# Optimization experiments

Measured on AMD Instinct MI355X. Metric: run time of the kernel, lower is better.

The kernel has to match this reference:

```python
import jax, jax.numpy as jnp
import numpy as np
from jax import lax

DYADIC_ORDER = 0
NAIVE_SOLVER = False


def _increments(X, Y):
    # Linear static kernel Gram: (A, M, N)
    G = jnp.einsum('amd,and->amn', X, Y)
    # Second-order finite-difference increments: (A, M-1, N-1)
    inc = G[:, 1:, 1:] + G[:, :-1, :-1] - G[:, 1:, :-1] - G[:, :-1, 1:]
    f = 2 ** DYADIC_ORDER
    if f > 1:
        # torch `tile` with index_select == consecutive repeat == jnp.repeat
        inc = jnp.repeat(jnp.repeat(inc, f, axis=1), f, axis=2) / float(f * f)
    return inc


def _sig_kernel(X, Y):
    """Signature-kernel PDE solve. X:(A,M,D), Y:(A,N,D) -> (A,)"""
    inc = _increments(X, Y)            # (A, MM, NN)
    A, MM, NN = inc.shape

    def row_step(prev_row, g_row):
        # prev_row: (A, NN+1) = K[i, :];  g_row: (A, NN) = G[:, i, :]
        def col_step(k_left, inp):
            k00, k01, g = inp          # each (A,)
            if NAIVE_SOLVER:
                k_new = k_left + k01 + k00 * (g - 1.0)
            else:
                k_new = (k_left + k01) * (1.0 + 0.5 * g + g * g / 12.0) \
                        - k00 * (1.0 - g * g / 12.0)
            return k_new, k_new

        xs = (prev_row[:, :-1].T, prev_row[:, 1:].T, g_row.T)  # (NN, A) each
        _, tail = lax.scan(col_step, jnp.ones((A,), inc.dtype), xs)
        new_row = jnp.concatenate([jnp.ones((A, 1), inc.dtype), tail.T], axis=1)
        return new_row, None

    init_row = jnp.ones((A, NN + 1), inc.dtype)  # K[0, :] = 1
    final_row, _ = lax.scan(row_step, init_row, jnp.moveaxis(inc, 1, 0))
    return final_row[:, -1]            # K[:, MM, NN]


def setup_inputs() -> dict:
    key = jax.random.key(0)
    kx, ky = jax.random.split(key)
    A, M, D = 128, 256, 16
    # scale 0.1 keeps Gram increments small so the PDE stays stable
    X = 0.1 * jax.random.normal(kx, (A, M, D), dtype=jnp.float32)
    Y = 0.1 * jax.random.normal(ky, (A, M, D), dtype=jnp.float32)
    return {"X": X, "Y": Y}


def reference(X, Y):
    k_XX = _sig_kernel(X, X)
    k_YY = _sig_kernel(Y, Y)
    k_XY = _sig_kernel(X, Y)
    return jnp.mean(k_XX) + jnp.mean(k_YY) - 2.0 * jnp.mean(k_XY)
```

## Files before the change

### kernel.cpp

```cpp
#include <hip/hip_runtime.h>

typedef float f32x2 __attribute__((ext_vector_type(2)));

#define NA   128
#define NPTS 256
#define DD   16
#define MMI  255
#define NSTEP (MMI + 63)

__device__ __forceinline__ float wave_shr1(float x, float boundary) {
    int r = __builtin_amdgcn_update_dpp(
        __builtin_bit_cast(int, boundary),
        __builtin_bit_cast(int, x),
        0x138 , 0xF, 0xF, false);
    return __builtin_bit_cast(float, r);
}

__global__ __launch_bounds__(64)
void sig_pde(const float* __restrict__ X, const float* __restrict__ Y,
             float* __restrict__ out) {
    const int pid  = blockIdx.x;
    const int pair = pid >> 7;
    const int a    = pid & 127;
    const float* U = (pair == 1) ? Y : X;
    const float* V = (pair == 0) ? X : Y;
    const float  w = (pair == 2) ? (-2.0f / (float)NA) : (1.0f / (float)NA);
    U += (size_t)a * (NPTS * DD);
    V += (size_t)a * (NPTS * DD);

    __shared__ float dU[4][256][4];

    const int lane = threadIdx.x;

    const float4* U4 = (const float4*)U;
    #pragma unroll
    for (int i = 0; i < 16; ++i) {
        int t  = lane + (i << 6);
        int qd = t >> 8;
        int r  = t & 255;
        float4 val = make_float4(0.f, 0.f, 0.f, 0.f);
        if (r < MMI) {
            float4 lo = U4[r * 4 + qd];
            float4 hi = U4[r * 4 + 4 + qd];
            val = make_float4(hi.x - lo.x, hi.y - lo.y, hi.z - lo.z, hi.w - lo.w);
        }
        *(float4*)(&dU[qd][r][0]) = val;
    }

    f32x2 v[4][8];
    #pragma unroll
    for (int k = 0; k < 4; ++k) {
        int j = (lane << 2) + k;
        const bool valid = (j < MMI);
        const int jj = valid ? j : 0;
        const float2* Va = (const float2*)(V + (size_t)jj * DD);
        const float2* Vb = (const float2*)(V + (size_t)(jj + 1) * DD);
        #pragma unroll
        for (int q = 0; q < 8; ++q) {
            float2 lo = Va[q], hi = Vb[q];
            v[k][q] = valid ? f32x2{hi.x - lo.x, hi.y - lo.y} : f32x2{0.f, 0.f};
        }
    }

    __syncthreads();

    auto rowidx = [&](int s) {
        int rr = s - lane;
        return ((unsigned)rr < (unsigned)MMI) ? rr : 255;
    };
    auto load_row = [&](int s, f32x2* uu) {
        const float4* p = (const float4*)&dU[0][rowidx(s)][0];
        #pragma unroll
        for (int q = 0; q < 4; ++q) {
            float4 t = p[q << 8];
            uu[2 * q + 0] = f32x2{t.x, t.y};
            uu[2 * q + 1] = f32x2{t.z, t.w};
        }
    };

    float c1[4], c2[4];
    auto compute_c = [&](const f32x2* uu) {
        #pragma unroll
        for (int k = 0; k < 4; ++k) {
            f32x2 acc = uu[0] * v[k][0];
            #pragma unroll
            for (int q = 1; q < 8; ++q) acc += uu[q] * v[k][q];
            const float g = acc.x + acc.y;
            const float e = g * g * (1.0f / 12.0f);
            c1[k] = fmaf(0.5f, g, 1.0f) + e;
            c2[k] = 1.0f - e;
        }
    };

    float kup0 = 1.f, kup1 = 1.f, kup2 = 1.f, kup3 = 1.f;
    float shnew = 1.f, shprev = 1.f;

    auto step = [&]() {
        const float left   = shnew;
        const float upleft = shprev;
        const float pre0 = fmaf(kup0, c1[0], -(upleft * c2[0]));
        const float pre1 = fmaf(kup1, c1[1], -(kup0 * c2[1]));
        const float pre2 = fmaf(kup2, c1[2], -(kup1 * c2[2]));
        const float pre3 = fmaf(kup3, c1[3], -(kup2 * c2[3]));
        const float t0 = fmaf(left, c1[0], pre0);
        const float t1 = fmaf(t0,   c1[1], pre1);
        const float t2 = fmaf(t1,   c1[2], pre2);
        const float t3 = fmaf(t2,   c1[3], pre3);
        shprev = shnew;
        kup0 = t0; kup1 = t1; kup2 = t2; kup3 = t3;
        shnew = wave_shr1(t3, 1.0f);
    };

    f32x2 bufA[8], bufB[8], bufC[8];
    {
        f32x2 t[8];
        load_row(0, t);
        compute_c(t);
    }
    load_row(1, bufA);
    load_row(2, bufB);

    for (int s = 0; s < NSTEP; s += 3) {
        load_row(s + 3, bufC);
        step();
        compute_c(bufA);

        load_row(s + 4, bufA);
        step();
        compute_c(bufB);

        load_row(s + 5, bufB);
        step();
        compute_c(bufC);
    }

    if (lane == 63) atomicAdd(out, w * kup2);
}

extern "C" void kernel_launch(void* const* d_in, const int* in_sizes, int n_in,
                              void* d_out, int out_size, void* d_ws, size_t ws_size,
                              hipStream_t stream) {
    const float* X = (const float*)d_in[0];
    const float* Y = (const float*)d_in[1];
    float* out = (float*)d_out;
    hipMemsetAsync(out, 0, sizeof(float), stream);
    sig_pde<<<dim3(3 * NA), dim3(64), 0, stream>>>(X, Y, out);
}
```

Baseline: 112.5 us.

## Precompute skewed Gram increments in fp16 workspace before the PDE sweep

Splits the work into two kernels. A parallel kernel computes all Gram increments in anti-diagonal (skewed) order and stores them as fp16 in the workspace. A lean wavefront kernel then streams them from global memory with a 6-deep prefetch, so the serial PDE loop no longer does the 16-wide dot products. This trades an extra kernel launch and global memory traffic for a shorter serial critical path. Storing increments in fp16 adds precision risk, and the original single kernel remains as a fallback when the workspace is too small.

```diff
diff --git a/kernel.cpp b/kernel.cpp
--- a/kernel.cpp
+++ b/kernel.cpp
@@ -1,12 +1,16 @@
 #include <hip/hip_runtime.h>
+#include <hip/hip_fp16.h>
 
 typedef float f32x2 __attribute__((ext_vector_type(2)));
 
-#define NA   128
-#define NPTS 256
-#define DD   16
-#define MMI  255
-#define NSTEP (MMI + 63)
+#define NA    128
+#define NPTS  256
+#define DD    16
+#define MMI   255
+#define NSTEP 318
+#define GROWS 318
+#define G_ELEMS ((size_t)3 * NA * GROWS * 256)
+#define G_BYTES (G_ELEMS * 2)
 
 __device__ __forceinline__ float wave_shr1(float x, float boundary) {
     int r = __builtin_amdgcn_update_dpp(
@@ -14,6 +18,137 @@
         __builtin_bit_cast(int, x),
         0x138 , 0xF, 0xF, false);
     return __builtin_bit_cast(float, r);
+}
+
+__global__ __launch_bounds__(256)
+void sig_gram(const float* __restrict__ X, const float* __restrict__ Y,
+              __half* __restrict__ G) {
+    const int bx    = blockIdx.x;
+    const int pb    = bx >> 2;
+    const int chunk = bx & 3;
+    const int pair  = pb >> 7;
+    const int a     = pb & 127;
+    const float* U = (pair == 1) ? Y : X;
+    const float* V = (pair == 0) ? X : Y;
+    U += (size_t)a * (NPTS * DD);
+    V += (size_t)a * (NPTS * DD);
+
+    __shared__ float dU[4][256][4];
+    __shared__ float dV[4][256][4];
+
+    const int tid = threadIdx.x;
+
+    const float4* U4 = (const float4*)U;
+    const float4* V4 = (const float4*)V;
+    #pragma unroll
+    for (int q = 0; q < 4; ++q) {
+        float4 uval = make_float4(0.f, 0.f, 0.f, 0.f);
+        float4 vval = make_float4(0.f, 0.f, 0.f, 0.f);
+        if (tid < MMI) {
+            float4 lo = U4[tid * 4 + q], hi = U4[tid * 4 + 4 + q];
+            uval = make_float4(hi.x - lo.x, hi.y - lo.y, hi.z - lo.z, hi.w - lo.w);
+            lo = V4[tid * 4 + q]; hi = V4[tid * 4 + 4 + q];
+            vval = make_float4(hi.x - lo.x, hi.y - lo.y, hi.z - lo.z, hi.w - lo.w);
+        }
+        *(float4*)(&dU[q][tid][0]) = uval;
+        *(float4*)(&dV[q][tid][0]) = vval;
+    }
+    __syncthreads();
+
+    f32x2 v[8];
+    #pragma unroll
+    for (int q = 0; q < 4; ++q) {
+        float4 t = *(const float4*)(&dV[q][tid][0]);
+        v[2 * q + 0] = f32x2{t.x, t.y};
+        v[2 * q + 1] = f32x2{t.z, t.w};
+    }
+
+    const int s0beg = 80 * chunk;
+    const int s0end = (s0beg + 80 < GROWS) ? s0beg + 80 : GROWS;
+    int rr = s0beg - (tid >> 2);
+    __half* gp = G + (size_t)pb * (GROWS * 256) + (size_t)s0beg * 256 + tid;
+
+    for (int s0 = s0beg; s0 < s0end; ++s0) {
+        int rc = rr < 0 ? 0 : (rr > 255 ? 255 : rr);
+        f32x2 acc;
+        {
+            float4 t0 = *(const float4*)(&dU[0][rc][0]);
+            float4 t1 = *(const float4*)(&dU[1][rc][0]);
+            float4 t2 = *(const float4*)(&dU[2][rc][0]);
+            float4 t3 = *(const float4*)(&dU[3][rc][0]);
+            acc = f32x2{t0.x, t0.y} * v[0];
+            acc = __builtin_elementwise_fma(f32x2{t0.z, t0.w}, v[1], acc);
+            acc = __builtin_elementwise_fma(f32x2{t1.x, t1.y}, v[2], acc);
+            acc = __builtin_elementwise_fma(f32x2{t1.z, t1.w}, v[3], acc);
+            acc = __builtin_elementwise_fma(f32x2{t2.x, t2.y}, v[4], acc);
+            acc = __builtin_elementwise_fma(f32x2{t2.z, t2.w}, v[5], acc);
+            acc = __builtin_elementwise_fma(f32x2{t3.x, t3.y}, v[6], acc);
+            acc = __builtin_elementwise_fma(f32x2{t3.z, t3.w}, v[7], acc);
+        }
+        float g = acc.x + acc.y;
+        g = (rr < 0) ? 0.f : g;
+        *gp = __float2half(g);
+        gp += 256;
+        ++rr;
+    }
+}
+
+__global__ __launch_bounds__(64)
+void sig_pde2(const __half* __restrict__ G, float* __restrict__ out) {
+    const int pid  = blockIdx.x;
+    const int pair = pid >> 7;
+    const float w  = (pair == 2) ? (-2.0f / (float)NA) : (1.0f / (float)NA);
+    const int lane = threadIdx.x;
+
+    const __half* gp = G + (size_t)pid * (GROWS * 256) + 4 * lane;
+
+    float kup0 = 1.f, kup1 = 1.f, kup2 = 1.f, kup3 = 1.f;
+    float shnew = 1.f, shprev = 1.f;
+
+    auto LOADK = [&](int k) { return *(const uint2*)(gp + k * 256); };
+
+    auto STEP = [&](uint2 b) {
+        float2 f01 = __half22float2(__builtin_bit_cast(__half2, b.x));
+        float2 f23 = __half22float2(__builtin_bit_cast(__half2, b.y));
+        f32x2 g01 = f32x2{f01.x, f01.y}, g23 = f32x2{f23.x, f23.y};
+        f32x2 e01 = (g01 * g01) * f32x2{1.f / 12.f, 1.f / 12.f};
+        f32x2 e23 = (g23 * g23) * f32x2{1.f / 12.f, 1.f / 12.f};
+        f32x2 c1a = __builtin_elementwise_fma(g01, f32x2{0.5f, 0.5f},
+                                              f32x2{1.f, 1.f}) + e01;
+        f32x2 c1b = __builtin_elementwise_fma(g23, f32x2{0.5f, 0.5f},
+                                              f32x2{1.f, 1.f}) + e23;
+        f32x2 c2a = f32x2{1.f, 1.f} - e01;
+        f32x2 c2b = f32x2{1.f, 1.f} - e23;
+
+        const float left = shnew, upleft = shprev;
+        const float pre0 = fmaf(kup0, c1a.x, -(upleft * c2a.x));
+        const float pre1 = fmaf(kup1, c1a.y, -(kup0 * c2a.y));
+        const float pre2 = fmaf(kup2, c1b.x, -(kup1 * c2b.x));
+        const float pre3 = fmaf(kup3, c1b.y, -(kup2 * c2b.y));
+        const float t0 = fmaf(left, c1a.x, pre0);
+        const float t1 = fmaf(t0,   c1a.y, pre1);
+        const float t2 = fmaf(t1,   c1b.x, pre2);
+        const float t3 = fmaf(t2,   c1b.y, pre3);
+        shprev = shnew;
+        kup0 = t0; kup1 = t1; kup2 = t2; kup3 = t3;
+        shnew = wave_shr1(t3, 1.0f);
+    };
+
+    uint2 b0 = LOADK(0), b1 = LOADK(1), b2 = LOADK(2),
+          b3 = LOADK(3), b4 = LOADK(4), b5 = LOADK(5);
+    gp += 6 * 256;
+    for (int it = 0; it < 52; ++it) {
+        STEP(b0); b0 = LOADK(0);
+        STEP(b1); b1 = LOADK(1);
+        STEP(b2); b2 = LOADK(2);
+        STEP(b3); b3 = LOADK(3);
+        STEP(b4); b4 = LOADK(4);
+        STEP(b5); b5 = LOADK(5);
+        gp += 6 * 256;
+    }
+    STEP(b0); STEP(b1); STEP(b2); STEP(b3); STEP(b4); STEP(b5);
+
+    if (lane == 63) atomicAdd(out, w * kup2);
 }
 
 __global__ __launch_bounds__(64)
@@ -27,26 +162,20 @@
     const float  w = (pair == 2) ? (-2.0f / (float)NA) : (1.0f / (float)NA);
     U += (size_t)a * (NPTS * DD);
     V += (size_t)a * (NPTS * DD);
-
     __shared__ float dU[4][256][4];
-
     const int lane = threadIdx.x;
-
     const float4* U4 = (const float4*)U;
     #pragma unroll
     for (int i = 0; i < 16; ++i) {
-        int t  = lane + (i << 6);
-        int qd = t >> 8;
-        int r  = t & 255;
+        int t = lane + (i << 6);
+        int qd = t >> 8, r = t & 255;
         float4 val = make_float4(0.f, 0.f, 0.f, 0.f);
         if (r < MMI) {
-            float4 lo = U4[r * 4 + qd];
-            float4 hi = U4[r * 4 + 4 + qd];
+            float4 lo = U4[r * 4 + qd], hi = U4[r * 4 + 4 + qd];
             val = make_float4(hi.x - lo.x, hi.y - lo.y, hi.z - lo.z, hi.w - lo.w);
         }
         *(float4*)(&dU[qd][r][0]) = val;
     }
-
     f32x2 v[4][8];
     #pragma unroll
     for (int k = 0; k < 4; ++k) {
@@ -61,9 +190,7 @@
             v[k][q] = valid ? f32x2{hi.x - lo.x, hi.y - lo.y} : f32x2{0.f, 0.f};
         }
     }
-
     __syncthreads();
-
     auto rowidx = [&](int s) {
         int rr = s - lane;
         return ((unsigned)rr < (unsigned)MMI) ? rr : 255;
@@ -77,7 +204,6 @@
             uu[2 * q + 1] = f32x2{t.z, t.w};
         }
     };
-
     float c1[4], c2[4];
     auto compute_c = [&](const f32x2* uu) {
         #pragma unroll
@@ -91,13 +217,10 @@
             c2[k] = 1.0f - e;
         }
     };
-
     float kup0 = 1.f, kup1 = 1.f, kup2 = 1.f, kup3 = 1.f;
     float shnew = 1.f, shprev = 1.f;
-
     auto step = [&]() {
-        const float left   = shnew;
-        const float upleft = shprev;
+        const float left = shnew, upleft = shprev;
         const float pre0 = fmaf(kup0, c1[0], -(upleft * c2[0]));
         const float pre1 = fmaf(kup1, c1[1], -(kup0 * c2[1]));
         const float pre2 = fmaf(kup2, c1[2], -(kup1 * c2[2]));
@@ -110,7 +233,6 @@
         kup0 = t0; kup1 = t1; kup2 = t2; kup3 = t3;
         shnew = wave_shr1(t3, 1.0f);
     };
-
     f32x2 bufA[8], bufB[8], bufC[8];
     {
         f32x2 t[8];
@@ -119,21 +241,11 @@
     }
     load_row(1, bufA);
     load_row(2, bufB);
-
     for (int s = 0; s < NSTEP; s += 3) {
-        load_row(s + 3, bufC);
-        step();
-        compute_c(bufA);
-
-        load_row(s + 4, bufA);
-        step();
-        compute_c(bufB);
-
-        load_row(s + 5, bufB);
-        step();
-        compute_c(bufC);
-    }
-
+        load_row(s + 3, bufC); step(); compute_c(bufA);
+        load_row(s + 4, bufA); step(); compute_c(bufB);
+        load_row(s + 5, bufB); step(); compute_c(bufC);
+    }
     if (lane == 63) atomicAdd(out, w * kup2);
 }
 
@@ -144,5 +256,11 @@
     const float* Y = (const float*)d_in[1];
     float* out = (float*)d_out;
     hipMemsetAsync(out, 0, sizeof(float), stream);
-    sig_pde<<<dim3(3 * NA), dim3(64), 0, stream>>>(X, Y, out);
-}
+    if (ws_size >= G_BYTES) {
+        __half* G = (__half*)d_ws;
+        sig_gram<<<dim3(3 * NA * 4), dim3(256), 0, stream>>>(X, Y, G);
+        sig_pde2<<<dim3(3 * NA), dim3(64), 0, stream>>>(G, out);
+    } else {
+        sig_pde<<<dim3(3 * NA), dim3(64), 0, stream>>>(X, Y, out);
+    }
+}
```

Measured after the change: 122.0 us. 8.4% more time.

## Split Gram increment production and PDE sweep into producer/consumer waves via LDS ring

Applied to the files above, without the earlier changes.

The block grows from one wave to four. Three producer waves compute the Gram increments for upcoming anti-diagonals and write them as fp16 into a shared-memory ring buffer. A single consumer wave reads batches of 16 and runs the serial wavefront recurrence, with the two sides synchronised per phase by __syncthreads. The intent is to take the dot-product work off the critical serial dependency chain. The risks are barrier overhead each phase, lower precision in the increments from fp16 storage, and fewer concurrent blocks per CU because of the larger block and LDS footprint.

```diff
diff --git a/kernel.cpp b/kernel.cpp
--- a/kernel.cpp
+++ b/kernel.cpp
@@ -1,12 +1,14 @@
 #include <hip/hip_runtime.h>
+#include <hip/hip_fp16.h>
 
 typedef float f32x2 __attribute__((ext_vector_type(2)));
 
-#define NA   128
-#define NPTS 256
-#define DD   16
-#define MMI  255
-#define NSTEP (MMI + 63)
+#define NA    128
+#define NPTS  256
+#define DD    16
+#define MMI   255
+#define NSTEP 318
+#define RING  96
 
 __device__ __forceinline__ float wave_shr1(float x, float boundary) {
     int r = __builtin_amdgcn_update_dpp(
@@ -16,9 +18,9 @@
     return __builtin_bit_cast(float, r);
 }
 
-__global__ __launch_bounds__(64)
-void sig_pde(const float* __restrict__ X, const float* __restrict__ Y,
-             float* __restrict__ out) {
+__global__ __launch_bounds__(256)
+void sig_fused(const float* __restrict__ X, const float* __restrict__ Y,
+               float* __restrict__ out) {
     const int pid  = blockIdx.x;
     const int pair = pid >> 7;
     const int a    = pid & 127;
@@ -28,113 +30,156 @@
     U += (size_t)a * (NPTS * DD);
     V += (size_t)a * (NPTS * DD);
 
-    __shared__ float dU[4][256][4];
+    __shared__ float  dU[256][16];
+    __shared__ __half ring[RING][256];
 
-    const int lane = threadIdx.x;
+    const int tid  = threadIdx.x;
+    const int wid  = tid >> 6;
+    const int lane = tid & 63;
 
-    const float4* U4 = (const float4*)U;
-    #pragma unroll
-    for (int i = 0; i < 16; ++i) {
-        int t  = lane + (i << 6);
-        int qd = t >> 8;
-        int r  = t & 255;
-        float4 val = make_float4(0.f, 0.f, 0.f, 0.f);
-        if (r < MMI) {
-            float4 lo = U4[r * 4 + qd];
-            float4 hi = U4[r * 4 + 4 + qd];
-            val = make_float4(hi.x - lo.x, hi.y - lo.y, hi.z - lo.z, hi.w - lo.w);
+    {
+        const float4* U4 = (const float4*)U;
+        #pragma unroll
+        for (int m = 0; m < 4; ++m) {
+            int idx = tid + 256 * m;
+            int row = idx >> 2;
+            float4 val = make_float4(0.f, 0.f, 0.f, 0.f);
+            if (row < MMI) {
+                float4 lo = U4[idx];
+                float4 hi = U4[idx + 4];
+                val = make_float4(hi.x - lo.x, hi.y - lo.y,
+                                  hi.z - lo.z, hi.w - lo.w);
+            }
+            *(float4*)(&dU[row][(idx & 3) * 4]) = val;
         }
-        *(float4*)(&dU[qd][r][0]) = val;
+    }
+    {
+        float4* rp = (float4*)&ring[0][0];
+        const float4 z = make_float4(0.f, 0.f, 0.f, 0.f);
+        #pragma unroll
+        for (int m = 0; m < 12; ++m) rp[tid + 256 * m] = z;
     }
 
-    f32x2 v[4][8];
-    #pragma unroll
-    for (int k = 0; k < 4; ++k) {
-        int j = (lane << 2) + k;
-        const bool valid = (j < MMI);
-        const int jj = valid ? j : 0;
-        const float2* Va = (const float2*)(V + (size_t)jj * DD);
-        const float2* Vb = (const float2*)(V + (size_t)(jj + 1) * DD);
+    f32x2 dv[4][8];
+    if (wid != 0) {
         #pragma unroll
-        for (int q = 0; q < 8; ++q) {
-            float2 lo = Va[q], hi = Vb[q];
-            v[k][q] = valid ? f32x2{hi.x - lo.x, hi.y - lo.y} : f32x2{0.f, 0.f};
+        for (int k = 0; k < 4; ++k) {
+            int j = 4 * lane + k;
+            const bool valid = (j < MMI);
+            const int jj = valid ? j : 0;
+            const float2* Va = (const float2*)(V + (size_t)jj * DD);
+            const float2* Vb = (const float2*)(V + (size_t)(jj + 1) * DD);
+            #pragma unroll
+            for (int q = 0; q < 8; ++q) {
+                float2 lo = Va[q], hi = Vb[q];
+                dv[k][q] = valid ? f32x2{hi.x - lo.x, hi.y - lo.y}
+                                 : f32x2{0.f, 0.f};
+            }
         }
     }
-
     __syncthreads();
 
-    auto rowidx = [&](int s) {
-        int rr = s - lane;
-        return ((unsigned)rr < (unsigned)MMI) ? rr : 255;
-    };
-    auto load_row = [&](int s, f32x2* uu) {
-        const float4* p = (const float4*)&dU[0][rowidx(s)][0];
-        #pragma unroll
-        for (int q = 0; q < 4; ++q) {
-            float4 t = p[q << 8];
-            uu[2 * q + 0] = f32x2{t.x, t.y};
-            uu[2 * q + 1] = f32x2{t.z, t.w};
+    auto produce = [&](int r) {
+        int slot = r + lane;
+        slot -= (slot >= 96)  ? 96 : 0;
+        slot -= (slot >= 96)  ? 96 : 0;
+        slot -= (slot >= 96)  ? 96 : 0;
+        uint2 wv = make_uint2(0u, 0u);
+        if (r < MMI) {
+            const float4* up4 = (const float4*)&dU[r][0];
+            float4 u0 = up4[0], u1 = up4[1], u2 = up4[2], u3 = up4[3];
+            f32x2 uu[8] = {
+                f32x2{u0.x, u0.y}, f32x2{u0.z, u0.w},
+                f32x2{u1.x, u1.y}, f32x2{u1.z, u1.w},
+                f32x2{u2.x, u2.y}, f32x2{u2.z, u2.w},
+                f32x2{u3.x, u3.y}, f32x2{u3.z, u3.w}};
+            f32x2 a0 = uu[0] * dv[0][0];
+            f32x2 a1 = uu[0] * dv[1][0];
+            f32x2 a2 = uu[0] * dv[2][0];
+            f32x2 a3 = uu[0] * dv[3][0];
+            #pragma unroll
+            for (int q = 1; q < 8; ++q) {
+                a0 = __builtin_elementwise_fma(uu[q], dv[0][q], a0);
+                a1 = __builtin_elementwise_fma(uu[q], dv[1][q], a1);
+                a2 = __builtin_elementwise_fma(uu[q], dv[2][q], a2);
+                a3 = __builtin_elementwise_fma(uu[q], dv[3][q], a3);
+            }
+            __half2 h01 = __floats2half2_rn(a0.x + a0.y, a1.x + a1.y);
+            __half2 h23 = __floats2half2_rn(a2.x + a2.y, a3.x + a3.y);
+            wv.x = __builtin_bit_cast(unsigned int, h01);
+            wv.y = __builtin_bit_cast(unsigned int, h23);
         }
-    };
-
-    float c1[4], c2[4];
-    auto compute_c = [&](const f32x2* uu) {
-        #pragma unroll
-        for (int k = 0; k < 4; ++k) {
-            f32x2 acc = uu[0] * v[k][0];
-            #pragma unroll
-            for (int q = 1; q < 8; ++q) acc += uu[q] * v[k][q];
-            const float g = acc.x + acc.y;
-            const float e = g * g * (1.0f / 12.0f);
-            c1[k] = fmaf(0.5f, g, 1.0f) + e;
-            c2[k] = 1.0f - e;
-        }
+        *(uint2*)(&ring[slot][4 * lane]) = wv;
     };
 
     float kup0 = 1.f, kup1 = 1.f, kup2 = 1.f, kup3 = 1.f;
     float shnew = 1.f, shprev = 1.f;
 
-    auto step = [&]() {
-        const float left   = shnew;
-        const float upleft = shprev;
-        const float pre0 = fmaf(kup0, c1[0], -(upleft * c2[0]));
-        const float pre1 = fmaf(kup1, c1[1], -(kup0 * c2[1]));
-        const float pre2 = fmaf(kup2, c1[2], -(kup1 * c2[2]));
-        const float pre3 = fmaf(kup3, c1[3], -(kup2 * c2[3]));
-        const float t0 = fmaf(left, c1[0], pre0);
-        const float t1 = fmaf(t0,   c1[1], pre1);
-        const float t2 = fmaf(t1,   c1[2], pre2);
-        const float t3 = fmaf(t2,   c1[3], pre3);
+    auto STEP = [&](uint2 b) {
+        float2 f01 = __half22float2(__builtin_bit_cast(__half2, b.x));
+        float2 f23 = __half22float2(__builtin_bit_cast(__half2, b.y));
+        f32x2 g01 = f32x2{f01.x, f01.y}, g23 = f32x2{f23.x, f23.y};
+        f32x2 e01 = (g01 * g01) * f32x2{1.f/12.f, 1.f/12.f};
+        f32x2 e23 = (g23 * g23) * f32x2{1.f/12.f, 1.f/12.f};
+        f32x2 c1a = __builtin_elementwise_fma(g01, f32x2{0.5f, 0.5f},
+                                              f32x2{1.f, 1.f}) + e01;
+        f32x2 c1b = __builtin_elementwise_fma(g23, f32x2{0.5f, 0.5f},
+                                              f32x2{1.f, 1.f}) + e23;
+        f32x2 c2a = f32x2{1.f, 1.f} - e01;
+        f32x2 c2b = f32x2{1.f, 1.f} - e23;
+        const float left = shnew, upleft = shprev;
+        const float pre0 = fmaf(kup0, c1a.x, -(upleft * c2a.x));
+        const float pre1 = fmaf(kup1, c1a.y, -(kup0 * c2a.y));
+        const float pre2 = fmaf(kup2, c1b.x, -(kup1 * c2b.x));
+        const float pre3 = fmaf(kup3, c1b.y, -(kup2 * c2b.y));
+        const float t0 = fmaf(left, c1a.x, pre0);
+        const float t1 = fmaf(t0,   c1a.y, pre1);
+        const float t2 = fmaf(t1,   c1b.x, pre2);
+        const float t3 = fmaf(t2,   c1b.y, pre3);
         shprev = shnew;
         kup0 = t0; kup1 = t1; kup2 = t2; kup3 = t3;
         shnew = wave_shr1(t3, 1.0f);
     };
 
-    f32x2 bufA[8], bufB[8], bufC[8];
-    {
-        f32x2 t[8];
-        load_row(0, t);
-        compute_c(t);
+    if (wid != 0) {
+        for (int i = wid - 1; i < 16; i += 3) produce(i);
     }
-    load_row(1, bufA);
-    load_row(2, bufB);
+    __syncthreads();
 
-    for (int s = 0; s < NSTEP; s += 3) {
-        load_row(s + 3, bufC);
-        step();
-        compute_c(bufA);
-
-        load_row(s + 4, bufA);
-        step();
-        compute_c(bufB);
-
-        load_row(s + 5, bufB);
-        step();
-        compute_c(bufC);
+    for (int ph = 0; ph < 19; ++ph) {
+        if (wid == 0) {
+            int slot0 = (16 * ph) % 96;
+            uint2 gb[16];
+            #pragma unroll
+            for (int i = 0; i < 16; ++i) {
+                int sl = slot0 + i;
+                sl -= (sl >= 96) ? 96 : 0;
+                gb[i] = *(const uint2*)(&ring[sl][4 * lane]);
+            }
+            #pragma unroll
+            for (int i = 0; i < 16; ++i) STEP(gb[i]);
+        } else {
+            for (int i = wid - 1; i < 16; i += 3) {
+                int r = 16 * ph + 16 + i;
+                if (r < NSTEP) produce(r);
+            }
+        }
+        __syncthreads();
     }
 
-    if (lane == 63) atomicAdd(out, w * kup2);
+    if (wid == 0) {
+        const int slot0 = 304 % 96;
+        uint2 gb[14];
+        #pragma unroll
+        for (int i = 0; i < 14; ++i) {
+            int sl = slot0 + i;
+            sl -= (sl >= 96) ? 96 : 0;
+            gb[i] = *(const uint2*)(&ring[sl][4 * lane]);
+        }
+        #pragma unroll
+        for (int i = 0; i < 14; ++i) STEP(gb[i]);
+        if (lane == 63) atomicAdd(out, w * kup2);
+    }
 }
 
 extern "C" void kernel_launch(void* const* d_in, const int* in_sizes, int n_in,
@@ -144,5 +189,5 @@
     const float* Y = (const float*)d_in[1];
     float* out = (float*)d_out;
     hipMemsetAsync(out, 0, sizeof(float), stream);
-    sig_pde<<<dim3(3 * NA), dim3(64), 0, stream>>>(X, Y, out);
+    sig_fused<<<dim3(3 * NA), dim3(256), 0, stream>>>(X, Y, out);
 }
```

Result: faster. 100.2 us (-10.9%).
